# Performance work log

Measured on AMD Instinct MI355X. Metric: run time of the kernel, lower is better.

Reference implementation:

```python
import jax, jax.numpy as jnp
import numpy as np

NUM_GRAPHS = 1024

def setup_inputs() -> dict:
    key = jax.random.key(0)
    ks = jax.random.split(key, 6)
    N, E = 500000, 16000000
    x = jax.random.normal(ks[0], (N, 4), dtype=jnp.float32)
    edge_index = jax.random.randint(ks[1], (2, E), 0, N, dtype=jnp.int32)
    batch = jnp.sort(jax.random.randint(ks[2], (N,), 0, NUM_GRAPHS, dtype=jnp.int32))
    eps = jnp.zeros((), dtype=jnp.float32)
    W1 = jax.random.normal(ks[3], (4, 16), dtype=jnp.float32) * 0.5
    b1 = jnp.zeros((16,), dtype=jnp.float32)
    W2 = jax.random.normal(ks[4], (16, 4), dtype=jnp.float32) * 0.25
    b2 = jnp.zeros((4,), dtype=jnp.float32)
    return {"x": x, "edge_index": edge_index, "batch": batch,
            "eps": eps, "W1": W1, "b1": b1, "W2": W2, "b2": b2}

def reference(x, edge_index, batch, eps, W1, b1, W2, b2):
    N = x.shape[0]
    src, dst = edge_index[0], edge_index[1]
    # GINConv aggregation: sum of neighbor (source) features at each target node
    agg = jax.ops.segment_sum(x[src], dst, num_segments=N)  # [N, 4]
    h = (1.0 + eps) * x + agg
    # 2-layer MLP: Lin(4,16) -> ReLU -> Lin(16,4)
    h = jax.nn.relu(h @ W1 + b1) @ W2 + b2
    h = jax.nn.relu(h)
    # global_mean_pool over batch segment ids
    sums = jax.ops.segment_sum(h, batch, num_segments=NUM_GRAPHS)      # [G, 4]
    cnts = jax.ops.segment_sum(jnp.ones((N,), h.dtype), batch, num_segments=NUM_GRAPHS)
    pooled = sums / jnp.maximum(cnts, 1.0)[:, None]
    return jax.nn.log_softmax(pooled, axis=1)
```

## Files before the change

kernel.cpp:

```cpp
#include <hip/hip_runtime.h>

#define NUM_GRAPHS 1024
#define BIN_BITS 10
#define BIN_SIZE (1 << BIN_BITS)
#define EB 4096
#define STH 512
#define EPT 8
#define CURS 16
#define ACCTH 256
#define ACCW 4

typedef int v4i __attribute__((ext_vector_type(4)));

__device__ inline unsigned bf16_rn(float f) {
    unsigned u = __float_as_uint(f);
    return (u + 0x7FFFu + ((u >> 16) & 1u)) >> 16;
}
__global__ void prep_kernel(const float4* __restrict__ x, uint2* __restrict__ x16,
                            int N, int* __restrict__ cursor,
                            float* __restrict__ gsum, float* __restrict__ gcnt,
                            int cap) {
    int i = blockIdx.x * blockDim.x + threadIdx.x;
    if (i < 512) cursor[i * CURS] = i * cap;
    if (i < NUM_GRAPHS * 4) gsum[i] = 0.0f;
    if (i < NUM_GRAPHS) gcnt[i] = 0.0f;
    if (i < N) {
        float4 v = x[i];
        uint2 r;
        r.x = bf16_rn(v.x) | (bf16_rn(v.y) << 16);
        r.y = bf16_rn(v.z) | (bf16_rn(v.w) << 16);
        x16[i] = r;
    }
}

__global__ void __launch_bounds__(STH) bin_scatter(const int* __restrict__ src,
                                                   const int* __restrict__ dst,
                                                   int* __restrict__ packed,
                                                   int* __restrict__ cursor,
                                                   int E, int cap, int nb) {
    __shared__ int shist[512];
    __shared__ int sgb[512];

    const int t = threadIdx.x;
    const int b0 = blockIdx.x * EB;
    const int myBase = b0 + t * EPT;

    for (int j = t; j < 512; j += STH) shist[j] = 0;
    __syncthreads();

    int pv[EPT];
    int bl[EPT];
    const bool full = (myBase + EPT <= E);
    if (full) {
#pragma unroll
        for (int v = 0; v < EPT / 4; ++v) {
            int4 d = *(const int4*)(dst + myBase + v * 4);
            int4 s = *(const int4*)(src + myBase + v * 4);
            int bn, lp;
            bn = ((unsigned)d.x) >> BIN_BITS; lp = atomicAdd(&shist[bn], 1);
            pv[v * 4 + 0] = ((d.x & (BIN_SIZE - 1)) << 19) | s.x;
            bl[v * 4 + 0] = (bn << 13) | lp;
            bn = ((unsigned)d.y) >> BIN_BITS; lp = atomicAdd(&shist[bn], 1);
            pv[v * 4 + 1] = ((d.y & (BIN_SIZE - 1)) << 19) | s.y;
            bl[v * 4 + 1] = (bn << 13) | lp;
            bn = ((unsigned)d.z) >> BIN_BITS; lp = atomicAdd(&shist[bn], 1);
            pv[v * 4 + 2] = ((d.z & (BIN_SIZE - 1)) << 19) | s.z;
            bl[v * 4 + 2] = (bn << 13) | lp;
            bn = ((unsigned)d.w) >> BIN_BITS; lp = atomicAdd(&shist[bn], 1);
            pv[v * 4 + 3] = ((d.w & (BIN_SIZE - 1)) << 19) | s.w;
            bl[v * 4 + 3] = (bn << 13) | lp;
        }
    } else {
#pragma unroll
        for (int i = 0; i < EPT; ++i) {
            int e = myBase + i;
            bool ok = e < E;
            int d = ok ? dst[e] : 0;
            int s = ok ? src[e] : 0;
            int bn = ((unsigned)d) >> BIN_BITS;
            int lp = 0;
            if (ok) lp = atomicAdd(&shist[bn], 1);
            pv[i] = ((d & (BIN_SIZE - 1)) << 19) | s;
            bl[i] = ok ? ((bn << 13) | lp) : -1;
        }
    }
    __syncthreads();

    if (t < nb) {
        int c = shist[t];
        sgb[t] = (c > 0) ? atomicAdd(&cursor[t * CURS], c) : 0;
    }
    __syncthreads();

    if (full) {
#pragma unroll
        for (int i = 0; i < EPT; ++i) {
            int bn = ((unsigned)bl[i]) >> 13;
            int lp = bl[i] & 0x1FFF;
            int pos = sgb[bn] + lp;
            if (pos < (bn + 1) * cap)
                packed[pos] = pv[i];
        }
    } else {
#pragma unroll
        for (int i = 0; i < EPT; ++i) {
            if (bl[i] >= 0) {
                int bn = ((unsigned)bl[i]) >> 13;
                int lp = bl[i] & 0x1FFF;
                int pos = sgb[bn] + lp;
                if (pos < (bn + 1) * cap)
                    packed[pos] = pv[i];
            }
        }
    }
}

__global__ void __launch_bounds__(ACCTH) bin_accum_mlp_pool(
        const float4* __restrict__ x,
        const uint2* __restrict__ x16,
        const int* __restrict__ packed,
        const int* __restrict__ cursor,
        const int* __restrict__ batch,
        const float* __restrict__ eps_p,
        const float* __restrict__ W1, const float* __restrict__ b1,
        const float* __restrict__ W2, const float* __restrict__ b2,
        float* __restrict__ gsum, float* __restrict__ gcnt,
        int N, int cap) {
    __shared__ float planes[ACCW][BIN_SIZE][4];

    const int bin = blockIdx.x;
    const int t = threadIdx.x;
    const int lane = t & 63;
    const int wave = t >> 6;

    {
        float4* pz = (float4*)&planes[0][0][0];
        float4 z; z.x = 0.f; z.y = 0.f; z.z = 0.f; z.w = 0.f;
#pragma unroll
        for (int i = 0; i < 16; ++i) pz[t + i * ACCTH] = z;
    }
    __syncthreads();

    const int start = bin * cap;
    int end = cursor[bin * CURS];
    if (end > start + cap) end = start + cap;
    int cnt = end - start; if (cnt < 0) cnt = 0;

    int seg = ((cnt + ACCW - 1) / ACCW + 3) & ~3;
    int s0 = start + wave * seg;
    int s1 = s0 + seg; if (s1 > end) s1 = end;

    for (int base = s0; base < s1; base += 256) {
        int b = base + lane * 4;
        int pe[4];
        if (b + 3 < s1) {
            v4i p4 = __builtin_nontemporal_load((const v4i*)(packed + b));
            pe[0] = p4.x; pe[1] = p4.y; pe[2] = p4.z; pe[3] = p4.w;
        } else {
            pe[0] = (b + 0 < s1) ? packed[b + 0] : -1;
            pe[1] = (b + 1 < s1) ? packed[b + 1] : -1;
            pe[2] = (b + 2 < s1) ? packed[b + 2] : -1;
            pe[3] = (b + 3 < s1) ? packed[b + 3] : -1;
        }
        uint2 g[4];
#pragma unroll
        for (int k = 0; k < 4; ++k) g[k] = x16[pe[k] & 0x7FFFF];

#pragma unroll
        for (int k = 0; k < 4; ++k) {
            int p = pe[k];
            bool ok = p >= 0;
            int dl = (((unsigned)p) >> 19) & (BIN_SIZE - 1);
            unsigned long long m;
            {
                unsigned long long bv = __ballot(ok);
                m = ok ? bv : ~bv;
#pragma unroll
                for (int bb = 0; bb < BIN_BITS; ++bb) {
                    unsigned long long bl_ = __ballot((dl >> bb) & 1);
                    m &= ((dl >> bb) & 1) ? bl_ : ~bl_;
                }
            }
            int rank = ok ? (int)__popcll(m & ((1ull << lane) - 1ull)) : -1;

            float v0 = __uint_as_float(g[k].x << 16);
            float v1 = __uint_as_float(g[k].x & 0xFFFF0000u);
            float v2 = __uint_as_float(g[k].y << 16);
            float v3 = __uint_as_float(g[k].y & 0xFFFF0000u);
            float4* pp = (float4*)&planes[wave][dl][0];
            for (int pass = 0; __any(rank >= pass); ++pass) {
                if (rank == pass) {
                    float4 a = *pp;
                    a.x += v0; a.y += v1; a.z += v2; a.w += v3;
                    *pp = a;
                }
            }
        }
    }
    __syncthreads();

    const float eps = eps_p[0];
    for (int half = 0; half < 4; ++half) {
        int node = t + half * ACCTH;
        float4 a = *(const float4*)&planes[0][node][0];
#pragma unroll
        for (int w = 1; w < ACCW; ++w) {
            float4 bq = *(const float4*)&planes[w][node][0];
            a.x += bq.x; a.y += bq.y; a.z += bq.z; a.w += bq.w;
        }

        int n = bin * BIN_SIZE + node;
        bool valid = n < N;
        float o0 = 0.f, o1 = 0.f, o2 = 0.f, o3 = 0.f;
        int g = -1;
        if (valid) {
            float4 xv = x[n];
            float h0 = (1.0f + eps) * xv.x + a.x;
            float h1 = (1.0f + eps) * xv.y + a.y;
            float h2 = (1.0f + eps) * xv.z + a.z;
            float h3 = (1.0f + eps) * xv.w + a.w;

            float tmp[16];
#pragma unroll
            for (int j = 0; j < 16; ++j) {
                float v = b1[j] + h0 * W1[j] + h1 * W1[16 + j] + h2 * W1[32 + j] + h3 * W1[48 + j];
                tmp[j] = v > 0.0f ? v : 0.0f;
            }
            float o[4];
#pragma unroll
            for (int j = 0; j < 4; ++j) {
                float v = b2[j];
#pragma unroll
                for (int k = 0; k < 16; ++k) v += tmp[k] * W2[k * 4 + j];
                o[j] = v > 0.0f ? v : 0.0f;
            }
            o0 = o[0]; o1 = o[1]; o2 = o[2]; o3 = o[3];
            g = batch[n];
        }

        int g0 = __shfl(g, 0);
        bool uni = __all(g == g0);
        if (uni && g0 >= 0) {
#pragma unroll
            for (int off = 32; off > 0; off >>= 1) {
                o0 += __shfl_down(o0, off);
                o1 += __shfl_down(o1, off);
                o2 += __shfl_down(o2, off);
                o3 += __shfl_down(o3, off);
            }
            if (lane == 0) {
                unsafeAtomicAdd(&gsum[(size_t)g0 * 4 + 0], o0);
                unsafeAtomicAdd(&gsum[(size_t)g0 * 4 + 1], o1);
                unsafeAtomicAdd(&gsum[(size_t)g0 * 4 + 2], o2);
                unsafeAtomicAdd(&gsum[(size_t)g0 * 4 + 3], o3);
                unsafeAtomicAdd(&gcnt[g0], 64.0f);
            }
        } else if (valid) {
            unsafeAtomicAdd(&gsum[(size_t)g * 4 + 0], o0);
            unsafeAtomicAdd(&gsum[(size_t)g * 4 + 1], o1);
            unsafeAtomicAdd(&gsum[(size_t)g * 4 + 2], o2);
            unsafeAtomicAdd(&gsum[(size_t)g * 4 + 3], o3);
            unsafeAtomicAdd(&gcnt[g], 1.0f);
        }
    }
}

__global__ void pool_softmax_kernel(const float* __restrict__ gsum,
                                    const float* __restrict__ gcnt,
                                    float* __restrict__ out) {
    int g = blockIdx.x * blockDim.x + threadIdx.x;
    if (g >= NUM_GRAPHS) return;
    float c = fmaxf(gcnt[g], 1.0f);
    float p0 = gsum[g * 4 + 0] / c;
    float p1 = gsum[g * 4 + 1] / c;
    float p2 = gsum[g * 4 + 2] / c;
    float p3 = gsum[g * 4 + 3] / c;
    float m = fmaxf(fmaxf(p0, p1), fmaxf(p2, p3));
    float s = expf(p0 - m) + expf(p1 - m) + expf(p2 - m) + expf(p3 - m);
    float lse = m + logf(s);
    out[g * 4 + 0] = p0 - lse;
    out[g * 4 + 1] = p1 - lse;
    out[g * 4 + 2] = p2 - lse;
    out[g * 4 + 3] = p3 - lse;
}

__global__ void edge_scatter_kernel(const float4* __restrict__ x,
                                    const int* __restrict__ src,
                                    const int* __restrict__ dst,
                                    float* __restrict__ agg,
                                    int E) {
    int t = blockIdx.x * blockDim.x + threadIdx.x;
    int e = t * 4;
    if (e + 3 < E) {
        int4 s = *(const int4*)(src + e);
        int4 d = *(const int4*)(dst + e);
        float4 xv;
        xv = x[s.x];
        unsafeAtomicAdd(&agg[(size_t)d.x * 4 + 0], xv.x);
        unsafeAtomicAdd(&agg[(size_t)d.x * 4 + 1], xv.y);
        unsafeAtomicAdd(&agg[(size_t)d.x * 4 + 2], xv.z);
        unsafeAtomicAdd(&agg[(size_t)d.x * 4 + 3], xv.w);
        xv = x[s.y];
        unsafeAtomicAdd(&agg[(size_t)d.y * 4 + 0], xv.x);
        unsafeAtomicAdd(&agg[(size_t)d.y * 4 + 1], xv.y);
        unsafeAtomicAdd(&agg[(size_t)d.y * 4 + 2], xv.z);
        unsafeAtomicAdd(&agg[(size_t)d.y * 4 + 3], xv.w);
        xv = x[s.z];
        unsafeAtomicAdd(&agg[(size_t)d.z * 4 + 0], xv.x);
        unsafeAtomicAdd(&agg[(size_t)d.z * 4 + 1], xv.y);
        unsafeAtomicAdd(&agg[(size_t)d.z * 4 + 2], xv.z);
        unsafeAtomicAdd(&agg[(size_t)d.z * 4 + 3], xv.w);
        xv = x[s.w];
        unsafeAtomicAdd(&agg[(size_t)d.w * 4 + 0], xv.x);
        unsafeAtomicAdd(&agg[(size_t)d.w * 4 + 1], xv.y);
        unsafeAtomicAdd(&agg[(size_t)d.w * 4 + 2], xv.z);
        unsafeAtomicAdd(&agg[(size_t)d.w * 4 + 3], xv.w);
    } else {
        for (int i = e; i < E; ++i) {
            int sv = src[i], dv = dst[i];
            float4 xv = x[sv];
            unsafeAtomicAdd(&agg[(size_t)dv * 4 + 0], xv.x);
            unsafeAtomicAdd(&agg[(size_t)dv * 4 + 1], xv.y);
            unsafeAtomicAdd(&agg[(size_t)dv * 4 + 2], xv.z);
            unsafeAtomicAdd(&agg[(size_t)dv * 4 + 3], xv.w);
        }
    }
}

__global__ void node_mlp_pool_kernel(const float4* __restrict__ x,
                                     const float4* __restrict__ agg,
                                     const int* __restrict__ batch,
                                     const float* __restrict__ eps_p,
                                     const float* __restrict__ W1,
                                     const float* __restrict__ b1,
                                     const float* __restrict__ W2,
                                     const float* __restrict__ b2,
                                     float* __restrict__ gsum,
                                     float* __restrict__ gcnt,
                                     int N) {
    int i = blockIdx.x * blockDim.x + threadIdx.x;
    bool valid = i < N;
    float o0 = 0.f, o1 = 0.f, o2 = 0.f, o3 = 0.f;
    int g = -1;
    if (valid) {
        float eps = eps_p[0];
        float4 xv = x[i];
        float4 av = agg[i];
        float h0 = (1.0f + eps) * xv.x + av.x;
        float h1 = (1.0f + eps) * xv.y + av.y;
        float h2 = (1.0f + eps) * xv.z + av.z;
        float h3 = (1.0f + eps) * xv.w + av.w;
        float tmp[16];
#pragma unroll
        for (int j = 0; j < 16; ++j) {
            float v = b1[j] + h0 * W1[j] + h1 * W1[16 + j] + h2 * W1[32 + j] + h3 * W1[48 + j];
            tmp[j] = v > 0.0f ? v : 0.0f;
        }
        float o[4];
#pragma unroll
        for (int j = 0; j < 4; ++j) {
            float v = b2[j];
#pragma unroll
            for (int k = 0; k < 16; ++k) v += tmp[k] * W2[k * 4 + j];
            o[j] = v > 0.0f ? v : 0.0f;
        }
        o0 = o[0]; o1 = o[1]; o2 = o[2]; o3 = o[3];
        g = batch[i];
    }
    int g0 = __shfl(g, 0);
    bool uni = __all(g == g0);
    if (uni && g0 >= 0) {
#pragma unroll
        for (int off = 32; off > 0; off >>= 1) {
            o0 += __shfl_down(o0, off);
            o1 += __shfl_down(o1, off);
            o2 += __shfl_down(o2, off);
            o3 += __shfl_down(o3, off);
        }
        if ((threadIdx.x & 63) == 0) {
            unsafeAtomicAdd(&gsum[(size_t)g0 * 4 + 0], o0);
            unsafeAtomicAdd(&gsum[(size_t)g0 * 4 + 1], o1);
            unsafeAtomicAdd(&gsum[(size_t)g0 * 4 + 2], o2);
            unsafeAtomicAdd(&gsum[(size_t)g0 * 4 + 3], o3);
            unsafeAtomicAdd(&gcnt[g0], 64.0f);
        }
    } else if (valid) {
        unsafeAtomicAdd(&gsum[(size_t)g * 4 + 0], o0);
        unsafeAtomicAdd(&gsum[(size_t)g * 4 + 1], o1);
        unsafeAtomicAdd(&gsum[(size_t)g * 4 + 2], o2);
        unsafeAtomicAdd(&gsum[(size_t)g * 4 + 3], o3);
        unsafeAtomicAdd(&gcnt[g], 1.0f);
    }
}

extern "C" void kernel_launch(void* const* d_in, const int* in_sizes, int n_in,
                              void* d_out, int out_size, void* d_ws, size_t ws_size,
                              hipStream_t stream) {
    const float* x     = (const float*)d_in[0];
    const int*   ei    = (const int*)d_in[1];
    const int*   batch = (const int*)d_in[2];
    const float* eps   = (const float*)d_in[3];
    const float* W1    = (const float*)d_in[4];
    const float* b1    = (const float*)d_in[5];
    const float* W2    = (const float*)d_in[6];
    const float* b2    = (const float*)d_in[7];

    const int N = in_sizes[0] / 4;
    const int E = in_sizes[1] / 2;
    const int* src = ei;
    const int* dst = ei + (size_t)E;

    const int nb = (N + BIN_SIZE - 1) >> BIN_BITS;
    const int epb = (E + nb - 1) / nb;
    int cap = epb + epb / 8 + 1024;
    cap = (cap + 3) & ~3;

    size_t x16_elems = ((size_t)2 * N + 3) & ~(size_t)3;
    size_t packed_elems = ((size_t)nb * cap + 3) & ~(size_t)3;
    size_t need = (x16_elems + packed_elems + 512 * CURS + NUM_GRAPHS * 5) * sizeof(float);

    if (nb <= 512 && N < (1 << 19) && need <= ws_size) {
        uint2* x16    = (uint2*)d_ws;
        int*   packed = (int*)d_ws + x16_elems;
        int*   cursor = packed + packed_elems;
        float* gsum   = (float*)(cursor + 512 * CURS);
        float* gcnt   = gsum + (size_t)NUM_GRAPHS * 4;

        prep_kernel<<<(N + 511) / 512, 512, 0, stream>>>(
            (const float4*)x, x16, N, cursor, gsum, gcnt, cap);

        int nblocks_e = (E + EB - 1) / EB;
        bin_scatter<<<nblocks_e, STH, 0, stream>>>(src, dst, packed, cursor, E, cap, nb);

        bin_accum_mlp_pool<<<nb, ACCTH, 0, stream>>>(
            (const float4*)x, (const uint2*)x16, packed, cursor, batch, eps,
            W1, b1, W2, b2, gsum, gcnt, N, cap);

        pool_softmax_kernel<<<(NUM_GRAPHS + 255) / 256, 256, 0, stream>>>(
            gsum, gcnt, (float*)d_out);
    } else {
        float* agg  = (float*)d_ws;
        float* gsum = agg + (size_t)N * 4;
        float* gcnt = gsum + (size_t)NUM_GRAPHS * 4;
        size_t zero_bytes = ((size_t)N * 4 + NUM_GRAPHS * 5) * sizeof(float);
        (void)hipMemsetAsync(d_ws, 0, zero_bytes, stream);

        int e4 = (E + 3) / 4;
        edge_scatter_kernel<<<(e4 + 255) / 256, 256, 0, stream>>>(
            (const float4*)x, src, dst, agg, E);

        node_mlp_pool_kernel<<<(N + 255) / 256, 256, 0, stream>>>(
            (const float4*)x, (const float4*)agg, batch, eps, W1, b1, W2, b2,
            gsum, gcnt, N);

        pool_softmax_kernel<<<(NUM_GRAPHS + 255) / 256, 256, 0, stream>>>(
            gsum, gcnt, (float*)d_out);
    }
}
```

Before: 441.0 us.

## Replace LDS atomics in bin scatter with wave-level ballot match and per-wave histograms

The binning kernel no longer does a shared-memory atomicAdd per edge. Each wave finds lanes that share a bin through nine ballots over the bin bits, and the leader lane bumps a per-wave histogram. The per-wave counts are then prefix-summed per bin to get global offsets. It also adds an occupancy hint to launch bounds and uses nontemporal stores for the packed output. The cost is more ballot and ALU work and eight times the LDS for histograms.

```diff
diff --git a/kernel.cpp b/kernel.cpp
--- a/kernel.cpp
+++ b/kernel.cpp
@@ -6,6 +6,7 @@
 #define EB 4096
 #define STH 512
 #define EPT 8
+#define SWAVES 8
 #define CURS 16
 #define ACCTH 256
 #define ACCW 4
@@ -33,83 +34,95 @@
     }
 }
 
-__global__ void __launch_bounds__(STH) bin_scatter(const int* __restrict__ src,
-                                                   const int* __restrict__ dst,
-                                                   int* __restrict__ packed,
-                                                   int* __restrict__ cursor,
-                                                   int E, int cap, int nb) {
-    __shared__ int shist[512];
-    __shared__ int sgb[512];
+__global__ void __launch_bounds__(STH, 6) bin_scatter(const int* __restrict__ src,
+                                                      const int* __restrict__ dst,
+                                                      int* __restrict__ packed,
+                                                      int* __restrict__ cursor,
+                                                      int E, int cap, int nb) {
+    __shared__ int hist[SWAVES][512];
+    __shared__ int wbase[SWAVES][512];
 
     const int t = threadIdx.x;
+    const int lane = t & 63;
+    const int wave = t >> 6;
     const int b0 = blockIdx.x * EB;
     const int myBase = b0 + t * EPT;
 
-    for (int j = t; j < 512; j += STH) shist[j] = 0;
+    for (int j = t; j < SWAVES * 512; j += STH) (&hist[0][0])[j] = 0;
     __syncthreads();
 
-    int pv[EPT];
-    int bl[EPT];
+    int dbuf[EPT], sbuf[EPT];
     const bool full = (myBase + EPT <= E);
     if (full) {
-#pragma unroll
-        for (int v = 0; v < EPT / 4; ++v) {
-            int4 d = *(const int4*)(dst + myBase + v * 4);
-            int4 s = *(const int4*)(src + myBase + v * 4);
-            int bn, lp;
-            bn = ((unsigned)d.x) >> BIN_BITS; lp = atomicAdd(&shist[bn], 1);
-            pv[v * 4 + 0] = ((d.x & (BIN_SIZE - 1)) << 19) | s.x;
-            bl[v * 4 + 0] = (bn << 13) | lp;
-            bn = ((unsigned)d.y) >> BIN_BITS; lp = atomicAdd(&shist[bn], 1);
-            pv[v * 4 + 1] = ((d.y & (BIN_SIZE - 1)) << 19) | s.y;
-            bl[v * 4 + 1] = (bn << 13) | lp;
-            bn = ((unsigned)d.z) >> BIN_BITS; lp = atomicAdd(&shist[bn], 1);
-            pv[v * 4 + 2] = ((d.z & (BIN_SIZE - 1)) << 19) | s.z;
-            bl[v * 4 + 2] = (bn << 13) | lp;
-            bn = ((unsigned)d.w) >> BIN_BITS; lp = atomicAdd(&shist[bn], 1);
-            pv[v * 4 + 3] = ((d.w & (BIN_SIZE - 1)) << 19) | s.w;
-            bl[v * 4 + 3] = (bn << 13) | lp;
-        }
+        *(int4*)(dbuf)     = *(const int4*)(dst + myBase);
+        *(int4*)(dbuf + 4) = *(const int4*)(dst + myBase + 4);
+        *(int4*)(sbuf)     = *(const int4*)(src + myBase);
+        *(int4*)(sbuf + 4) = *(const int4*)(src + myBase + 4);
     } else {
 #pragma unroll
         for (int i = 0; i < EPT; ++i) {
             int e = myBase + i;
             bool ok = e < E;
-            int d = ok ? dst[e] : 0;
-            int s = ok ? src[e] : 0;
-            int bn = ((unsigned)d) >> BIN_BITS;
-            int lp = 0;
-            if (ok) lp = atomicAdd(&shist[bn], 1);
-            pv[i] = ((d & (BIN_SIZE - 1)) << 19) | s;
-            bl[i] = ok ? ((bn << 13) | lp) : -1;
-        }
+            dbuf[i] = ok ? dst[e] : 0;
+            sbuf[i] = ok ? src[e] : 0;
+        }
+    }
+
+    int pv[EPT];
+    int bnlp[EPT];
+#pragma unroll
+    for (int k = 0; k < EPT; ++k) {
+        int e = myBase + k;
+        bool ok = full || (e < E);
+        int d = dbuf[k];
+        int bn = ((unsigned)d) >> BIN_BITS;
+        pv[k] = ((d & (BIN_SIZE - 1)) << 19) | sbuf[k];
+        unsigned long long m = __ballot(ok);
+#pragma unroll
+        for (int bb = 0; bb < 9; ++bb) {
+            unsigned long long bm = __ballot((bn >> bb) & 1);
+            m &= ((bn >> bb) & 1) ? bm : ~bm;
+        }
+        int rank = (int)__popcll(m & ((1ull << lane) - 1ull));
+        int cnt  = (int)__popcll(m);
+        int leader = __ffsll((unsigned long long)m) - 1;
+        int old = hist[wave][bn];
+        if (ok && lane == leader) hist[wave][bn] = old + cnt;
+        bnlp[k] = ok ? ((bn << 16) | (old + rank)) : -1;
     }
     __syncthreads();
 
-    if (t < nb) {
-        int c = shist[t];
-        sgb[t] = (c > 0) ? atomicAdd(&cursor[t * CURS], c) : 0;
+    {
+        int c[SWAVES];
+        int total = 0;
+#pragma unroll
+        for (int w = 0; w < SWAVES; ++w) { c[w] = hist[w][t]; total += c[w]; }
+        int base = 0;
+        if (t < nb && total > 0) base = atomicAdd(&cursor[t * CURS], total);
+        int acc = base;
+#pragma unroll
+        for (int w = 0; w < SWAVES; ++w) { wbase[w][t] = acc; acc += c[w]; }
     }
     __syncthreads();
 
     if (full) {
 #pragma unroll
-        for (int i = 0; i < EPT; ++i) {
-            int bn = ((unsigned)bl[i]) >> 13;
-            int lp = bl[i] & 0x1FFF;
-            int pos = sgb[bn] + lp;
+        for (int k = 0; k < EPT; ++k) {
+            int bn = ((unsigned)bnlp[k]) >> 16;
+            int lp = bnlp[k] & 0xFFFF;
+            int pos = wbase[wave][bn] + lp;
             if (pos < (bn + 1) * cap)
-                packed[pos] = pv[i];
+                __builtin_nontemporal_store(pv[k], &packed[pos]);
         }
     } else {
 #pragma unroll
-        for (int i = 0; i < EPT; ++i) {
-            if (bl[i] >= 0) {
-                int bn = ((unsigned)bl[i]) >> 13;
-                int lp = bl[i] & 0x1FFF;
-                int pos = sgb[bn] + lp;
+        for (int k = 0; k < EPT; ++k) {
+            if (bnlp[k] >= 0) {
+                int bn = ((unsigned)bnlp[k]) >> 16;
+                int lp = bnlp[k] & 0xFFFF;
+                int pos = wbase[wave][bn] + lp;
                 if (pos < (bn + 1) * cap)
-                    packed[pos] = pv[i];
+                    __builtin_nontemporal_store(pv[k], &packed[pos]);
             }
         }
     }
```

Result: slower. 1.111 ms (+152.0%).
